# Optimization experiments

Hardware: AMD Instinct MI355X
Metric: run time of the kernel (lower is better)

Reference implementation:

```python
import jax, jax.numpy as jnp
import numpy as np

B, N, C, H = 8, 1024, 768, 12
D = C // H
SCALE = D ** -0.5


def setup_inputs() -> dict:
    key = jax.random.key(0)
    k1, k2, k3 = jax.random.split(key, 3)
    x = jax.random.normal(k1, (B, N, C), dtype=jnp.float32)
    w_qkv = jax.random.normal(k2, (C, 3 * C), dtype=jnp.float32) * (C ** -0.5)
    w_proj = jax.random.normal(k3, (C, C), dtype=jnp.float32) * (C ** -0.5)
    b_proj = jnp.zeros((C,), dtype=jnp.float32)
    return {"x": x, "w_qkv": w_qkv, "w_proj": w_proj, "b_proj": b_proj}


def reference(x, w_qkv, w_proj, b_proj):
    Bx, Nx, Cx = x.shape
    # qkv projection (no bias), split into q,k,v with shape [B, H, N, D]
    qkv = (x @ w_qkv).reshape(Bx, Nx, 3, H, D).transpose(2, 0, 3, 1, 4)
    q, k, v = qkv[0], qkv[1], qkv[2]
    # full attention matrix [B, H, N, N] (matches torch module's explicit materialization)
    attn = jnp.einsum('bhqd,bhkd->bhqk', q, k) * SCALE
    attn = jax.nn.softmax(attn, axis=-1)
    out = jnp.einsum('bhqk,bhkd->bhqd', attn, v)
    out = out.transpose(0, 2, 1, 3).reshape(Bx, Nx, Cx)
    return out @ w_proj + b_proj
```

## Files before the change

kernel.cpp:

```cpp
#include <hip/hip_runtime.h>


typedef unsigned short u16;
typedef short s16x8 __attribute__((ext_vector_type(8)));
typedef float f32x4 __attribute__((ext_vector_type(4)));
typedef u16   u16x8 __attribute__((ext_vector_type(8)));
typedef u16   u16x4 __attribute__((ext_vector_type(4)));

__device__ __forceinline__ u16 f2bf(float f) {
    unsigned int u = __builtin_bit_cast(unsigned int, f);
    u += 0x7FFFu + ((u >> 16) & 1u);
    return (u16)(u >> 16);
}

__device__ __forceinline__ void gload16(const u16* g, u16* l) {
    __builtin_amdgcn_global_load_lds(
        (const __attribute__((address_space(1))) unsigned int*)g,
        (__attribute__((address_space(3))) unsigned int*)l, 16, 0, 0);
}

__global__ __launch_bounds__(256) void prep(
    const float* __restrict__ x, u16* __restrict__ xb,
    const float* __restrict__ wq, u16* __restrict__ wqT,
    const float* __restrict__ wp, u16* __restrict__ wpT) {
    __shared__ float ts[32][33];
    const int g = blockIdx.x, tid = threadIdx.x;
    if (g < 3072) {
        const size_t i = ((size_t)g * 256 + tid) * 8;
        float4 v0 = *(const float4*)(x + i);
        float4 v1 = *(const float4*)(x + i + 4);
        u16x8 p;
        p[0] = f2bf(v0.x); p[1] = f2bf(v0.y); p[2] = f2bf(v0.z); p[3] = f2bf(v0.w);
        p[4] = f2bf(v1.x); p[5] = f2bf(v1.y); p[6] = f2bf(v1.z); p[7] = f2bf(v1.w);
        *(u16x8*)(xb + i) = p;
        return;
    }
    const float* in; u16* out; int K, Nc, n0, k0;
    if (g < 4800) {
        int gg = g - 3072; in = wq; out = wqT; K = 768; Nc = 2304;
        n0 = (gg % 72) * 32; k0 = (gg / 72) * 32;
    } else {
        int gg = g - 4800; in = wp; out = wpT; K = 768; Nc = 768;
        n0 = (gg % 24) * 32; k0 = (gg / 24) * 32;
    }
    const int tx = tid & 31, ty = tid >> 5;
#pragma unroll
    for (int j = 0; j < 4; ++j) {
        int r = ty + j * 8;
        ts[r][tx] = in[(size_t)(k0 + r) * Nc + n0 + tx];
    }
    __syncthreads();
#pragma unroll
    for (int j = 0; j < 4; ++j) {
        int r = ty + j * 8;
        out[(size_t)(n0 + r) * K + k0 + tx] = f2bf(ts[tx][r]);
    }
}

__global__ __launch_bounds__(256) void gemm_qkv(
    const u16* __restrict__ Aq, const u16* __restrict__ Bt,
    u16* __restrict__ qb, u16* __restrict__ kb, u16* __restrict__ vbT) {
    __shared__ __align__(16) u16 As[2][128 * 32];
    __shared__ __align__(16) u16 Bs[2][128 * 32];
    const int tid = threadIdx.x;
    const int lane = tid & 63, w = tid >> 6;
    const int m15 = lane & 15, quad = lane >> 4;
    const int wy = w >> 1, wx = w & 1;
    const int g = blockIdx.x;
    const int xcd = g & 7, s = g >> 3;
    const int yt = xcd * 8 + (s & 7), xt = s >> 3;
    const int m0 = yt * 128, n0 = xt * 128;
    const int srow16 = lane >> 2;
    const int scol = (lane & 3) * 8;

    f32x4 acc[4][4] = {};

    for (int k0 = 0; k0 < 768; k0 += 64) {
        __syncthreads();
#pragma unroll
        for (int j = 0; j < 2; ++j) {
            int rA = w * 32 + j * 16 + srow16;
            const u16* a0 = Aq + (size_t)(m0 + rA) * 768 + k0 + scol;
            const u16* b0 = Bt + (size_t)(n0 + rA) * 768 + k0 + scol;
            gload16(a0,      &As[0][(w * 32 + j * 16) * 32]);
            gload16(a0 + 32, &As[1][(w * 32 + j * 16) * 32]);
            gload16(b0,      &Bs[0][(w * 32 + j * 16) * 32]);
            gload16(b0 + 32, &Bs[1][(w * 32 + j * 16) * 32]);
        }
        __syncthreads();
#pragma unroll
        for (int h = 0; h < 2; ++h) {
            s16x8 av[4], bv[4];
#pragma unroll
            for (int ri = 0; ri < 4; ++ri)
                av[ri] = *(const s16x8*)&As[h][(wy * 64 + ri * 16 + m15) * 32 + quad * 8];
#pragma unroll
            for (int ci = 0; ci < 4; ++ci)
                bv[ci] = *(const s16x8*)&Bs[h][(wx * 64 + ci * 16 + m15) * 32 + quad * 8];
#pragma unroll
            for (int ri = 0; ri < 4; ++ri)
#pragma unroll
                for (int ci = 0; ci < 4; ++ci)
                    acc[ri][ci] = __builtin_amdgcn_mfma_f32_16x16x32_bf16(av[ri], bv[ci], acc[ri][ci], 0, 0, 0);
        }
    }

    const int which = xt / 6;
#pragma unroll
    for (int ri = 0; ri < 4; ++ri) {
        int mb = m0 + wy * 64 + ri * 16 + (quad << 2);
        int b = mb >> 10, row = mb & 1023;
#pragma unroll
        for (int ci = 0; ci < 4; ++ci) {
            int col = n0 + wx * 64 + ci * 16 + m15 - which * 768;
            int h = col >> 6, d = col & 63;
            size_t bhi = (size_t)(b * 12 + h);
            if (which == 2) {
                u16x4 pk;
#pragma unroll
                for (int rg = 0; rg < 4; ++rg) pk[rg] = f2bf(acc[ri][ci][rg]);
                *(u16x4*)&vbT[(bhi * 64 + d) * 1024 + row] = pk;
            } else {
                u16* dst = which ? kb : qb;
#pragma unroll
                for (int rg = 0; rg < 4; ++rg)
                    dst[(bhi * 1024 + row + rg) * 64 + d] = f2bf(acc[ri][ci][rg]);
            }
        }
    }
}

__global__ __launch_bounds__(256) void gemm_proj(
    const u16* __restrict__ A, const u16* __restrict__ Bt,
    const float* __restrict__ bias, float* __restrict__ out) {
    __shared__ __align__(16) u16 As[2][128 * 32];
    __shared__ __align__(16) u16 Bs[2][128 * 32];
    const int tid = threadIdx.x;
    const int lane = tid & 63, w = tid >> 6;
    const int m15 = lane & 15, quad = lane >> 4;
    const int wy = w >> 1, wx = w & 1;
    const int g = blockIdx.x;
    const int xcd = g & 7, s = g >> 3;
    const int yt = xcd * 8 + (s & 7), xt = s >> 3;
    const int m0 = yt * 128, n0 = xt * 128;
    const int srow16 = lane >> 2;
    const int scol = (lane & 3) * 8;

    f32x4 acc[4][4] = {};

    for (int k0 = 0; k0 < 768; k0 += 64) {
        __syncthreads();
#pragma unroll
        for (int j = 0; j < 2; ++j) {
            int rA = w * 32 + j * 16 + srow16;
            const u16* a0 = A  + (size_t)(m0 + rA) * 768 + k0 + scol;
            const u16* b0 = Bt + (size_t)(n0 + rA) * 768 + k0 + scol;
            gload16(a0,      &As[0][(w * 32 + j * 16) * 32]);
            gload16(a0 + 32, &As[1][(w * 32 + j * 16) * 32]);
            gload16(b0,      &Bs[0][(w * 32 + j * 16) * 32]);
            gload16(b0 + 32, &Bs[1][(w * 32 + j * 16) * 32]);
        }
        __syncthreads();
#pragma unroll
        for (int h = 0; h < 2; ++h) {
            s16x8 av[4], bv[4];
#pragma unroll
            for (int ri = 0; ri < 4; ++ri)
                av[ri] = *(const s16x8*)&As[h][(wy * 64 + ri * 16 + m15) * 32 + quad * 8];
#pragma unroll
            for (int ci = 0; ci < 4; ++ci)
                bv[ci] = *(const s16x8*)&Bs[h][(wx * 64 + ci * 16 + m15) * 32 + quad * 8];
#pragma unroll
            for (int ri = 0; ri < 4; ++ri)
#pragma unroll
                for (int ci = 0; ci < 4; ++ci)
                    acc[ri][ci] = __builtin_amdgcn_mfma_f32_16x16x32_bf16(av[ri], bv[ci], acc[ri][ci], 0, 0, 0);
        }
    }

#pragma unroll
    for (int ri = 0; ri < 4; ++ri) {
        int mb = m0 + wy * 64 + ri * 16 + (quad << 2);
#pragma unroll
        for (int ci = 0; ci < 4; ++ci) {
            int n = n0 + wx * 64 + ci * 16 + m15;
            float bv_ = bias[n];
#pragma unroll
            for (int rg = 0; rg < 4; ++rg)
                out[(size_t)(mb + rg) * 768 + n] = acc[ri][ci][rg] + bv_;
        }
    }
}

#define KS 72

__global__ __launch_bounds__(256) void attn_mfma(
    const u16* __restrict__ qb, const u16* __restrict__ kb,
    const u16* __restrict__ vbT, u16* __restrict__ aout) {
    __shared__ __align__(16) u16 Ks[64 * KS];
    __shared__ __align__(16) u16 Vs[64 * KS];
    __shared__ __align__(16) u16 Ps[8][16 * KS];
    const int tid = threadIdx.x, lane = tid & 63, w = tid >> 6;
    const int m15 = lane & 15, quad = lane >> 4;
    const int g = blockIdx.x;
    const int xcd = g & 7, s = g >> 3;
    const int bh = xcd * 12 + (s % 12);
    const int q0 = (s / 12) * 128;

    s16x8 aq[2][2];
#pragma unroll
    for (int qs = 0; qs < 2; ++qs) {
        const u16* qp = qb + ((size_t)bh * 1024 + q0 + w * 32 + qs * 16 + m15) * 64 + quad * 8;
        aq[qs][0] = *(const s16x8*)qp;
        aq[qs][1] = *(const s16x8*)(qp + 32);
    }

    s16x8 bones;
#pragma unroll
    for (int j = 0; j < 8; ++j) bones[j] = (m15 == 0) ? (short)0x3F80 : (short)0;

    f32x4 oacc[2][4] = {};
    f32x4 lacc[2] = {};

    const int srow = tid >> 2;
    const int soff = (tid & 3) * 16;
    const u16* kbase = kb + (size_t)bh * 1024 * 64;
    const u16* vbase = vbT + (size_t)bh * 64 * 1024;
    const float CE   = 0.125f * 1.44269504f;
    const float MOFF = 12.0f * 1.44269504f;

    for (int kt = 0; kt < 16; ++kt) {
        __syncthreads();
        const u16* kpp = kbase + ((size_t)kt * 64 + srow) * 64 + soff;
        const u16* vpp = vbase + (size_t)srow * 1024 + kt * 64 + soff;
        *(u16x8*)&Ks[srow * KS + soff]     = *(const u16x8*)kpp;
        *(u16x8*)&Ks[srow * KS + soff + 8] = *(const u16x8*)(kpp + 8);
        *(u16x8*)&Vs[srow * KS + soff]     = *(const u16x8*)vpp;
        *(u16x8*)&Vs[srow * KS + soff + 8] = *(const u16x8*)(vpp + 8);
        __syncthreads();

        f32x4 sacc[2][4] = {};
#pragma unroll
        for (int t = 0; t < 4; ++t)
#pragma unroll
            for (int ch = 0; ch < 2; ++ch) {
                s16x8 ak = *(const s16x8*)&Ks[(t * 16 + m15) * KS + quad * 8 + 32 * ch];
                sacc[0][t] = __builtin_amdgcn_mfma_f32_16x16x32_bf16(ak, aq[0][ch], sacc[0][t], 0, 0, 0);
                sacc[1][t] = __builtin_amdgcn_mfma_f32_16x16x32_bf16(ak, aq[1][ch], sacc[1][t], 0, 0, 0);
            }

#pragma unroll
        for (int qs = 0; qs < 2; ++qs)
#pragma unroll
            for (int t = 0; t < 4; ++t) {
                u16x4 pk;
#pragma unroll
                for (int reg = 0; reg < 4; ++reg) {
                    float pv = __builtin_amdgcn_exp2f(sacc[qs][t][reg] * CE - MOFF);
                    unsigned int u = __builtin_bit_cast(unsigned int, pv);
                    pk[reg] = (u16)(u >> 16);
                }
                *(u16x4*)&Ps[w * 2 + qs][m15 * KS + t * 16 + quad * 4] = pk;
            }

        s16x8 ap[2][2];
#pragma unroll
        for (int qs = 0; qs < 2; ++qs) {
            ap[qs][0] = *(const s16x8*)&Ps[w * 2 + qs][m15 * KS + quad * 8];
            ap[qs][1] = *(const s16x8*)&Ps[w * 2 + qs][m15 * KS + quad * 8 + 32];
#pragma unroll
            for (int ch = 0; ch < 2; ++ch)
                lacc[qs] = __builtin_amdgcn_mfma_f32_16x16x32_bf16(ap[qs][ch], bones, lacc[qs], 0, 0, 0);
        }
#pragma unroll
        for (int di = 0; di < 4; ++di)
#pragma unroll
            for (int ch = 0; ch < 2; ++ch) {
                s16x8 bv = *(const s16x8*)&Vs[(di * 16 + m15) * KS + quad * 8 + 32 * ch];
                oacc[0][di] = __builtin_amdgcn_mfma_f32_16x16x32_bf16(ap[0][ch], bv, oacc[0][di], 0, 0, 0);
                oacc[1][di] = __builtin_amdgcn_mfma_f32_16x16x32_bf16(ap[1][ch], bv, oacc[1][di], 0, 0, 0);
            }
    }

    const int b = bh / 12, h = bh - b * 12;
#pragma unroll
    for (int qs = 0; qs < 2; ++qs) {
        float linv[4];
#pragma unroll
        for (int reg = 0; reg < 4; ++reg)
            linv[reg] = 1.0f / __shfl(lacc[qs][reg], lane & 48);
#pragma unroll
        for (int di = 0; di < 4; ++di)
#pragma unroll
            for (int reg = 0; reg < 4; ++reg) {
                int q = q0 + w * 32 + qs * 16 + quad * 4 + reg;
                aout[((size_t)b * 1024 + q) * 768 + h * 64 + di * 16 + m15] =
                    f2bf(oacc[qs][di][reg] * linv[reg]);
            }
    }
}

extern "C" void kernel_launch(void* const* d_in, const int* in_sizes, int n_in,
                              void* d_out, int out_size, void* d_ws, size_t ws_size,
                              hipStream_t stream) {
    const float* x      = (const float*)d_in[0];
    const float* w_qkv  = (const float*)d_in[1];
    const float* w_proj = (const float*)d_in[2];
    const float* b_proj = (const float*)d_in[3];
    float* out = (float*)d_out;

    char* ws = (char*)d_ws;
    u16* wqkvT  = (u16*)ws;  ws += (size_t)2304 * 768 * 2;
    u16* wprojT = (u16*)ws;  ws += (size_t)768 * 768 * 2;
    u16* qb     = (u16*)ws;  ws += (size_t)96 * 1024 * 64 * 2;
    u16* kb     = (u16*)ws;  ws += (size_t)96 * 1024 * 64 * 2;
    u16* vbT    = (u16*)ws;  ws += (size_t)96 * 1024 * 64 * 2;
    u16* aout   = (u16*)ws;  ws += (size_t)8192 * 768 * 2;
    u16* xb     = aout;

    prep<<<dim3(5376), 256, 0, stream>>>(x, xb, w_qkv, wqkvT, w_proj, wprojT);
    gemm_qkv<<<dim3(1152), 256, 0, stream>>>(xb, wqkvT, qb, kb, vbT);
    attn_mfma<<<dim3(768), 256, 0, stream>>>(qb, kb, vbT, aout);
    gemm_proj<<<dim3(384), 256, 0, stream>>>(aout, wprojT, b_proj, out);
}
```

Baseline: 187.9 us.

## Rewrite QKV GEMM as 256x256 tile, 8-wave pipelined kernel with swizzled LDS

The QKV projection GEMM moves from 128x128 tiles with 4 waves to 256x256 tiles with 8 waves. The main loop is double-buffered and split into phases, with async global-to-LDS loads interleaved between MFMA bursts, explicit barriers and priority raising. LDS rows are XOR-swizzled to avoid bank conflicts. For Q and K the operands are swapped so stores can be packed 4-wide, aiming to cut LDS traffic, global load stalls and scalar stores. The trade-off is more LDS per block, heavy register use, and only 288 blocks, which may leave some CUs underused.

```diff
diff --git a/kernel.cpp b/kernel.cpp
--- a/kernel.cpp
+++ b/kernel.cpp
@@ -57,76 +57,167 @@
     }
 }
 
-__global__ __launch_bounds__(256) void gemm_qkv(
+template<bool SWAP, int NI>
+__device__ __forceinline__ void mfma_pair(f32x4 (&acc)[8][4], const s16x8 (&av)[8],
+                                          s16x8 bva, s16x8 bvb) {
+#pragma unroll
+    for (int mi = 0; mi < 8; ++mi) {
+        if (SWAP) {
+            acc[mi][NI]     = __builtin_amdgcn_mfma_f32_16x16x32_bf16(bva, av[mi], acc[mi][NI], 0, 0, 0);
+            acc[mi][NI + 1] = __builtin_amdgcn_mfma_f32_16x16x32_bf16(bvb, av[mi], acc[mi][NI + 1], 0, 0, 0);
+        } else {
+            acc[mi][NI]     = __builtin_amdgcn_mfma_f32_16x16x32_bf16(av[mi], bva, acc[mi][NI], 0, 0, 0);
+            acc[mi][NI + 1] = __builtin_amdgcn_mfma_f32_16x16x32_bf16(av[mi], bvb, acc[mi][NI + 1], 0, 0, 0);
+        }
+    }
+}
+
+#define PH_BAR()  asm volatile("s_barrier" ::: "memory")
+#define PH_LGKM() asm volatile("s_waitcnt lgkmcnt(0)" ::: "memory")
+
+template<bool SWAP>
+__device__ __forceinline__ void qkv_loop(f32x4 (&acc)[8][4],
+    const u16* __restrict__ Aq, const u16* __restrict__ Bt,
+    u16* As, u16* Bs, int m0, int n0, int lane, int w) {
+    const int m15 = lane & 15, quad = lane >> 4;
+    const int wy = w >> 2, wx = w & 3;
+    const int qsw8 = (quad ^ ((m15 >> 1) & 3)) * 8;
+    const int srow = lane >> 2;
+    const int scg = ((lane & 3) ^ ((lane >> 3) & 3)) * 8;
+    const int rg0 = w * 16, rg1 = (w + 8) * 16;
+    const size_t ga0 = (size_t)(m0 + rg0 + srow) * 768 + scg;
+    const size_t ga1 = (size_t)(m0 + rg1 + srow) * 768 + scg;
+    const size_t gb0 = (size_t)(n0 + rg0 + srow) * 768 + scg;
+    const size_t gb1 = (size_t)(n0 + rg1 + srow) * 768 + scg;
+
+    auto stA = [&](int buf, int ks, int t) {
+        const int k0 = t * 64 + ks * 32;
+        u16* dst = As + ((buf * 2 + ks) << 13);
+        gload16(Aq + ga0 + k0, dst + (rg0 << 5));
+        gload16(Aq + ga1 + k0, dst + (rg1 << 5));
+    };
+    auto stB = [&](int buf, int ks, int t) {
+        const int k0 = t * 64 + ks * 32;
+        u16* dst = Bs + ((buf * 2 + ks) << 13);
+        gload16(Bt + gb0 + k0, dst + (rg0 << 5));
+        gload16(Bt + gb1 + k0, dst + (rg1 << 5));
+    };
+
+    stA(0, 0, 0); stA(0, 1, 0); stB(0, 0, 0); stB(0, 1, 0);
+    stA(1, 0, 1); stA(1, 1, 1); stB(1, 0, 1);
+    asm volatile("s_waitcnt vmcnt(6)" ::: "memory");
+    PH_BAR();
+
+    const int arow = (wy * 128 + m15) * 32 + qsw8;
+    const int brow = (wx * 64 + m15) * 32 + qsw8;
+
+#pragma unroll 2
+    for (int t = 0; t < 12; ++t) {
+        const int cur = t & 1, nxt = cur ^ 1;
+        const int t1 = (t + 1 < 12) ? t + 1 : 0;
+        const int t2 = (t + 2 < 12) ? t + 2 : t - 10;
+        const u16* A0p = As + ((cur * 2 + 0) << 13);
+        const u16* A1p = As + ((cur * 2 + 1) << 13);
+        const u16* B0p = Bs + ((cur * 2 + 0) << 13);
+        const u16* B1p = Bs + ((cur * 2 + 1) << 13);
+        s16x8 av[8], bva, bvb;
+
+#pragma unroll
+        for (int mi = 0; mi < 8; ++mi)
+            av[mi] = *(const s16x8*)(A0p + arow + mi * 512);
+        bva = *(const s16x8*)(B0p + brow);
+        bvb = *(const s16x8*)(B0p + brow + 512);
+        stB(nxt, 1, t1);
+        PH_BAR(); PH_LGKM();
+        __builtin_amdgcn_s_setprio(1);
+        mfma_pair<SWAP, 0>(acc, av, bva, bvb);
+        __builtin_amdgcn_s_setprio(0);
+        PH_BAR();
+
+        bva = *(const s16x8*)(B0p + brow + 1024);
+        bvb = *(const s16x8*)(B0p + brow + 1536);
+        stA(cur, 0, t2);
+        PH_BAR(); PH_LGKM();
+        __builtin_amdgcn_s_setprio(1);
+        mfma_pair<SWAP, 2>(acc, av, bva, bvb);
+        __builtin_amdgcn_s_setprio(0);
+        PH_BAR();
+
+#pragma unroll
+        for (int mi = 0; mi < 8; ++mi)
+            av[mi] = *(const s16x8*)(A1p + arow + mi * 512);
+        bva = *(const s16x8*)(B1p + brow);
+        bvb = *(const s16x8*)(B1p + brow + 512);
+        stB(cur, 0, t2);
+        PH_BAR(); PH_LGKM();
+        __builtin_amdgcn_s_setprio(1);
+        mfma_pair<SWAP, 0>(acc, av, bva, bvb);
+        __builtin_amdgcn_s_setprio(0);
+        PH_BAR();
+
+        bva = *(const s16x8*)(B1p + brow + 1024);
+        bvb = *(const s16x8*)(B1p + brow + 1536);
+        stA(cur, 1, t2);
+        asm volatile("s_waitcnt vmcnt(6)" ::: "memory");
+        PH_BAR(); PH_LGKM();
+        __builtin_amdgcn_s_setprio(1);
+        mfma_pair<SWAP, 2>(acc, av, bva, bvb);
+        __builtin_amdgcn_s_setprio(0);
+        PH_BAR();
+    }
+    asm volatile("s_waitcnt vmcnt(0)" ::: "memory");
+}
+
+__global__ __launch_bounds__(512, 2) void gemm_qkv(
     const u16* __restrict__ Aq, const u16* __restrict__ Bt,
     u16* __restrict__ qb, u16* __restrict__ kb, u16* __restrict__ vbT) {
-    __shared__ __align__(16) u16 As[2][128 * 32];
-    __shared__ __align__(16) u16 Bs[2][128 * 32];
+    __shared__ __align__(16) u16 As[2 * 2 * 8192];
+    __shared__ __align__(16) u16 Bs[2 * 2 * 8192];
     const int tid = threadIdx.x;
     const int lane = tid & 63, w = tid >> 6;
     const int m15 = lane & 15, quad = lane >> 4;
-    const int wy = w >> 1, wx = w & 1;
-    const int g = blockIdx.x;
-    const int xcd = g & 7, s = g >> 3;
-    const int yt = xcd * 8 + (s & 7), xt = s >> 3;
-    const int m0 = yt * 128, n0 = xt * 128;
-    const int srow16 = lane >> 2;
-    const int scol = (lane & 3) * 8;
-
-    f32x4 acc[4][4] = {};
-
-    for (int k0 = 0; k0 < 768; k0 += 64) {
-        __syncthreads();
-#pragma unroll
-        for (int j = 0; j < 2; ++j) {
-            int rA = w * 32 + j * 16 + srow16;
-            const u16* a0 = Aq + (size_t)(m0 + rA) * 768 + k0 + scol;
-            const u16* b0 = Bt + (size_t)(n0 + rA) * 768 + k0 + scol;
-            gload16(a0,      &As[0][(w * 32 + j * 16) * 32]);
-            gload16(a0 + 32, &As[1][(w * 32 + j * 16) * 32]);
-            gload16(b0,      &Bs[0][(w * 32 + j * 16) * 32]);
-            gload16(b0 + 32, &Bs[1][(w * 32 + j * 16) * 32]);
-        }
-        __syncthreads();
-#pragma unroll
-        for (int h = 0; h < 2; ++h) {
-            s16x8 av[4], bv[4];
-#pragma unroll
-            for (int ri = 0; ri < 4; ++ri)
-                av[ri] = *(const s16x8*)&As[h][(wy * 64 + ri * 16 + m15) * 32 + quad * 8];
-#pragma unroll
-            for (int ci = 0; ci < 4; ++ci)
-                bv[ci] = *(const s16x8*)&Bs[h][(wx * 64 + ci * 16 + m15) * 32 + quad * 8];
-#pragma unroll
-            for (int ri = 0; ri < 4; ++ri)
-#pragma unroll
-                for (int ci = 0; ci < 4; ++ci)
-                    acc[ri][ci] = __builtin_amdgcn_mfma_f32_16x16x32_bf16(av[ri], bv[ci], acc[ri][ci], 0, 0, 0);
-        }
-    }
-
-    const int which = xt / 6;
-#pragma unroll
-    for (int ri = 0; ri < 4; ++ri) {
-        int mb = m0 + wy * 64 + ri * 16 + (quad << 2);
-        int b = mb >> 10, row = mb & 1023;
-#pragma unroll
-        for (int ci = 0; ci < 4; ++ci) {
-            int col = n0 + wx * 64 + ci * 16 + m15 - which * 768;
-            int h = col >> 6, d = col & 63;
-            size_t bhi = (size_t)(b * 12 + h);
-            if (which == 2) {
+    const int wy = w >> 2, wx = w & 3;
+    const int wg = (blockIdx.x & 7) * 36 + (blockIdx.x >> 3);
+    const int mt = wg / 9, nt = wg - mt * 9;
+    const int m0 = mt * 256, n0 = nt * 256;
+    const int which = nt / 3;
+
+    f32x4 acc[8][4] = {};
+    if (which < 2)
+        qkv_loop<true>(acc, Aq, Bt, As, Bs, m0, n0, lane, w);
+    else
+        qkv_loop<false>(acc, Aq, Bt, As, Bs, m0, n0, lane, w);
+
+    const int b  = (m0 + wy * 128) >> 10;
+    const int r0 = (m0 + wy * 128) & 1023;
+    const int n0p = n0 - which * 768;
+    const int h = (n0p + wx * 64) >> 6;
+    const size_t bhi = (size_t)(b * 12 + h);
+    if (which == 2) {
+#pragma unroll
+        for (int mi = 0; mi < 8; ++mi)
+#pragma unroll
+            for (int ni = 0; ni < 4; ++ni) {
                 u16x4 pk;
 #pragma unroll
-                for (int rg = 0; rg < 4; ++rg) pk[rg] = f2bf(acc[ri][ci][rg]);
-                *(u16x4*)&vbT[(bhi * 64 + d) * 1024 + row] = pk;
-            } else {
-                u16* dst = which ? kb : qb;
-#pragma unroll
-                for (int rg = 0; rg < 4; ++rg)
-                    dst[(bhi * 1024 + row + rg) * 64 + d] = f2bf(acc[ri][ci][rg]);
-            }
-        }
+                for (int rg = 0; rg < 4; ++rg) pk[rg] = f2bf(acc[mi][ni][rg]);
+                const int d = ni * 16 + m15;
+                const int tok = r0 + mi * 16 + (quad << 2);
+                *(u16x4*)&vbT[(bhi * 64 + d) * 1024 + tok] = pk;
+            }
+    } else {
+        u16* dst = which ? kb : qb;
+#pragma unroll
+        for (int mi = 0; mi < 8; ++mi)
+#pragma unroll
+            for (int ni = 0; ni < 4; ++ni) {
+                u16x4 pk;
+#pragma unroll
+                for (int rg = 0; rg < 4; ++rg) pk[rg] = f2bf(acc[mi][ni][rg]);
+                const int tok = r0 + mi * 16 + m15;
+                const int d = ni * 16 + (quad << 2);
+                *(u16x4*)&dst[(bhi * 1024 + tok) * 64 + d] = pk;
+            }
     }
 }
 
@@ -319,7 +410,7 @@
     u16* xb     = aout;
 
     prep<<<dim3(5376), 256, 0, stream>>>(x, xb, w_qkv, wqkvT, w_proj, wprojT);
-    gemm_qkv<<<dim3(1152), 256, 0, stream>>>(xb, wqkvT, qb, kb, vbT);
+    gemm_qkv<<<dim3(288), 512, 0, stream>>>(xb, wqkvT, qb, kb, vbT);
     attn_mfma<<<dim3(768), 256, 0, stream>>>(qb, kb, vbT, aout);
     gemm_proj<<<dim3(384), 256, 0, stream>>>(aout, wprojT, b_proj, out);
 }
```

New measurement: 205.4 us. 1.09x slower.

## Software-pipeline GEMM K-loop with swizzled LDS and vectorized Q/K stores

Applied to the files above, without the earlier changes.

Both projection GEMMs now share one K-loop that double-buffers 32-wide K slices. The next slice is prefetched via global_load_lds while MFMAs run on the current one, with a partial vmcnt wait and raw barriers replacing the two __syncthreads per iteration. LDS column groups are XOR-swizzled to reduce bank conflicts, and MFMA priority is raised around the compute block. For Q/K the MFMA operands are swapped so each lane holds four consecutive head-dim values, which lets the epilogue write 8-byte vector stores instead of scalar ones. Launch bounds now request 4 blocks per CU, which could cause register spills.

```diff
diff --git a/kernel.cpp b/kernel.cpp
--- a/kernel.cpp
+++ b/kernel.cpp
@@ -57,11 +57,67 @@
     }
 }
 
-__global__ __launch_bounds__(256) void gemm_qkv(
+template<bool SWAP>
+__device__ __forceinline__ void gemm_loop_128(
+    f32x4 (&acc)[4][4], const u16* __restrict__ A, const u16* __restrict__ B,
+    u16* As, u16* Bs, int m0, int n0, int lane, int w) {
+    const int m15 = lane & 15, quad = lane >> 4;
+    const int wy = w >> 1, wx = w & 1;
+    const int qsw8 = (quad ^ ((m15 >> 1) & 3)) * 8;
+    const int srow16 = lane >> 2;
+    const int scg = ((lane & 3) ^ ((lane >> 3) & 3)) * 8;
+    const size_t gA = (size_t)(m0 + w * 32 + srow16) * 768 + scg;
+    const size_t gB = (size_t)(n0 + w * 32 + srow16) * 768 + scg;
+
+    auto stage = [&](int buf, int s) {
+        const int k0 = (s < 24 ? s : 0) * 32;
+        u16* da = As + buf * 4096 + (w * 32) * 32;
+        u16* db = Bs + buf * 4096 + (w * 32) * 32;
+        gload16(A + gA + k0,            da);
+        gload16(A + gA + 16 * 768 + k0, da + 16 * 32);
+        gload16(B + gB + k0,            db);
+        gload16(B + gB + 16 * 768 + k0, db + 16 * 32);
+    };
+
+    stage(0, 0);
+    const int arow = (wy * 64 + m15) * 32 + qsw8;
+    const int brow = (wx * 64 + m15) * 32 + qsw8;
+
+#pragma unroll 2
+    for (int s = 0; s < 24; ++s) {
+        const int cur = s & 1;
+        stage(cur ^ 1, s + 1);
+        asm volatile("s_waitcnt vmcnt(4)" ::: "memory");
+        __builtin_amdgcn_s_barrier();
+        const u16* Ap = As + cur * 4096;
+        const u16* Bp = Bs + cur * 4096;
+        s16x8 av[4], bv[4];
+#pragma unroll
+        for (int ri = 0; ri < 4; ++ri)
+            av[ri] = *(const s16x8*)(Ap + arow + ri * 512);
+#pragma unroll
+        for (int ci = 0; ci < 4; ++ci)
+            bv[ci] = *(const s16x8*)(Bp + brow + ci * 512);
+        __builtin_amdgcn_s_setprio(1);
+#pragma unroll
+        for (int ri = 0; ri < 4; ++ri)
+#pragma unroll
+            for (int ci = 0; ci < 4; ++ci) {
+                if (SWAP)
+                    acc[ri][ci] = __builtin_amdgcn_mfma_f32_16x16x32_bf16(bv[ci], av[ri], acc[ri][ci], 0, 0, 0);
+                else
+                    acc[ri][ci] = __builtin_amdgcn_mfma_f32_16x16x32_bf16(av[ri], bv[ci], acc[ri][ci], 0, 0, 0);
+            }
+        __builtin_amdgcn_s_setprio(0);
+        __builtin_amdgcn_s_barrier();
+    }
+}
+
+__global__ __launch_bounds__(256, 4) void gemm_qkv(
     const u16* __restrict__ Aq, const u16* __restrict__ Bt,
     u16* __restrict__ qb, u16* __restrict__ kb, u16* __restrict__ vbT) {
-    __shared__ __align__(16) u16 As[2][128 * 32];
-    __shared__ __align__(16) u16 Bs[2][128 * 32];
+    __shared__ __align__(16) u16 As[2 * 128 * 32];
+    __shared__ __align__(16) u16 Bs[2 * 128 * 32];
     const int tid = threadIdx.x;
     const int lane = tid & 63, w = tid >> 6;
     const int m15 = lane & 15, quad = lane >> 4;
@@ -70,71 +126,52 @@
     const int xcd = g & 7, s = g >> 3;
     const int yt = xcd * 8 + (s & 7), xt = s >> 3;
     const int m0 = yt * 128, n0 = xt * 128;
-    const int srow16 = lane >> 2;
-    const int scol = (lane & 3) * 8;
+    const int which = xt / 6;
 
     f32x4 acc[4][4] = {};
-
-    for (int k0 = 0; k0 < 768; k0 += 64) {
-        __syncthreads();
-#pragma unroll
-        for (int j = 0; j < 2; ++j) {
-            int rA = w * 32 + j * 16 + srow16;
-            const u16* a0 = Aq + (size_t)(m0 + rA) * 768 + k0 + scol;
-            const u16* b0 = Bt + (size_t)(n0 + rA) * 768 + k0 + scol;
-            gload16(a0,      &As[0][(w * 32 + j * 16) * 32]);
-            gload16(a0 + 32, &As[1][(w * 32 + j * 16) * 32]);
-            gload16(b0,      &Bs[0][(w * 32 + j * 16) * 32]);
-            gload16(b0 + 32, &Bs[1][(w * 32 + j * 16) * 32]);
-        }
-        __syncthreads();
-#pragma unroll
-        for (int h = 0; h < 2; ++h) {
-            s16x8 av[4], bv[4];
-#pragma unroll
-            for (int ri = 0; ri < 4; ++ri)
-                av[ri] = *(const s16x8*)&As[h][(wy * 64 + ri * 16 + m15) * 32 + quad * 8];
-#pragma unroll
-            for (int ci = 0; ci < 4; ++ci)
-                bv[ci] = *(const s16x8*)&Bs[h][(wx * 64 + ci * 16 + m15) * 32 + quad * 8];
-#pragma unroll
-            for (int ri = 0; ri < 4; ++ri)
-#pragma unroll
-                for (int ci = 0; ci < 4; ++ci)
-                    acc[ri][ci] = __builtin_amdgcn_mfma_f32_16x16x32_bf16(av[ri], bv[ci], acc[ri][ci], 0, 0, 0);
-        }
-    }
-
-    const int which = xt / 6;
-#pragma unroll
-    for (int ri = 0; ri < 4; ++ri) {
-        int mb = m0 + wy * 64 + ri * 16 + (quad << 2);
-        int b = mb >> 10, row = mb & 1023;
-#pragma unroll
-        for (int ci = 0; ci < 4; ++ci) {
-            int col = n0 + wx * 64 + ci * 16 + m15 - which * 768;
-            int h = col >> 6, d = col & 63;
-            size_t bhi = (size_t)(b * 12 + h);
-            if (which == 2) {
+    if (which < 2)
+        gemm_loop_128<true >(acc, Aq, Bt, As, Bs, m0, n0, lane, w);
+    else
+        gemm_loop_128<false>(acc, Aq, Bt, As, Bs, m0, n0, lane, w);
+
+    const int b   = m0 >> 10;
+    const int r0  = (m0 & 1023) + wy * 64;
+    const int n0p = n0 - which * 768;
+    const int h   = (n0p >> 6) + wx;
+    const size_t bhi = (size_t)(b * 12 + h);
+    if (which == 2) {
+#pragma unroll
+        for (int ri = 0; ri < 4; ++ri)
+#pragma unroll
+            for (int ci = 0; ci < 4; ++ci) {
                 u16x4 pk;
 #pragma unroll
                 for (int rg = 0; rg < 4; ++rg) pk[rg] = f2bf(acc[ri][ci][rg]);
-                *(u16x4*)&vbT[(bhi * 64 + d) * 1024 + row] = pk;
-            } else {
-                u16* dst = which ? kb : qb;
-#pragma unroll
-                for (int rg = 0; rg < 4; ++rg)
-                    dst[(bhi * 1024 + row + rg) * 64 + d] = f2bf(acc[ri][ci][rg]);
-            }
-        }
-    }
-}
-
-__global__ __launch_bounds__(256) void gemm_proj(
+                const int d   = ci * 16 + m15;
+                const int tok = r0 + ri * 16 + (quad << 2);
+                *(u16x4*)&vbT[(bhi * 64 + d) * 1024 + tok] = pk;
+            }
+    } else {
+        u16* dst = which ? kb : qb;
+#pragma unroll
+        for (int ri = 0; ri < 4; ++ri)
+#pragma unroll
+            for (int ci = 0; ci < 4; ++ci) {
+                u16x4 pk;
+#pragma unroll
+                for (int rg = 0; rg < 4; ++rg) pk[rg] = f2bf(acc[ri][ci][rg]);
+                const int tok = r0 + ri * 16 + m15;
+                const int d   = ci * 16 + (quad << 2);
+                *(u16x4*)&dst[(bhi * 1024 + tok) * 64 + d] = pk;
+            }
+    }
+}
+
+__global__ __launch_bounds__(256, 4) void gemm_proj(
     const u16* __restrict__ A, const u16* __restrict__ Bt,
     const float* __restrict__ bias, float* __restrict__ out) {
-    __shared__ __align__(16) u16 As[2][128 * 32];
-    __shared__ __align__(16) u16 Bs[2][128 * 32];
+    __shared__ __align__(16) u16 As[2 * 128 * 32];
+    __shared__ __align__(16) u16 Bs[2 * 128 * 32];
     const int tid = threadIdx.x;
     const int lane = tid & 63, w = tid >> 6;
     const int m15 = lane & 15, quad = lane >> 4;
@@ -143,40 +180,9 @@
     const int xcd = g & 7, s = g >> 3;
     const int yt = xcd * 8 + (s & 7), xt = s >> 3;
     const int m0 = yt * 128, n0 = xt * 128;
-    const int srow16 = lane >> 2;
-    const int scol = (lane & 3) * 8;
 
     f32x4 acc[4][4] = {};
-
-    for (int k0 = 0; k0 < 768; k0 += 64) {
-        __syncthreads();
-#pragma unroll
-        for (int j = 0; j < 2; ++j) {
-            int rA = w * 32 + j * 16 + srow16;
-            const u16* a0 = A  + (size_t)(m0 + rA) * 768 + k0 + scol;
-            const u16* b0 = Bt + (size_t)(n0 + rA) * 768 + k0 + scol;
-            gload16(a0,      &As[0][(w * 32 + j * 16) * 32]);
-            gload16(a0 + 32, &As[1][(w * 32 + j * 16) * 32]);
-            gload16(b0,      &Bs[0][(w * 32 + j * 16) * 32]);
-            gload16(b0 + 32, &Bs[1][(w * 32 + j * 16) * 32]);
-        }
-        __syncthreads();
-#pragma unroll
-        for (int h = 0; h < 2; ++h) {
-            s16x8 av[4], bv[4];
-#pragma unroll
-            for (int ri = 0; ri < 4; ++ri)
-                av[ri] = *(const s16x8*)&As[h][(wy * 64 + ri * 16 + m15) * 32 + quad * 8];
-#pragma unroll
-            for (int ci = 0; ci < 4; ++ci)
-                bv[ci] = *(const s16x8*)&Bs[h][(wx * 64 + ci * 16 + m15) * 32 + quad * 8];
-#pragma unroll
-            for (int ri = 0; ri < 4; ++ri)
-#pragma unroll
-                for (int ci = 0; ci < 4; ++ci)
-                    acc[ri][ci] = __builtin_amdgcn_mfma_f32_16x16x32_bf16(av[ri], bv[ci], acc[ri][ci], 0, 0, 0);
-        }
-    }
+    gemm_loop_128<false>(acc, A, Bt, As, Bs, m0, n0, lane, w);
 
 #pragma unroll
     for (int ri = 0; ri < 4; ++ri) {
```

Result: no change. 190.1 us (+1.2%).
